# Optimization experiments

Hardware: AMD Instinct MI355X
Metric: run time of the kernel (lower is better)

The kernel has to match this reference:

```python
import jax, jax.numpy as jnp
import numpy as np

B, T, C, E, TOPK = 4, 4096, 1024, 8, 2
H = 4 * C

def setup_inputs() -> dict:
    key = jax.random.key(0)
    ks = jax.random.split(key, 8)
    s = 1.0 / np.sqrt(C)
    sh = 1.0 / np.sqrt(H)
    return {
        "x": jax.random.normal(ks[0], (B, T, C), jnp.float32),
        "noise_eps": jax.random.normal(ks[1], (B, T, E), jnp.float32),
        "route_w": jax.random.normal(ks[2], (C, E), jnp.float32) * s,
        "route_b": jnp.zeros((E,), jnp.float32),
        "noise_w": jax.random.normal(ks[3], (C, E), jnp.float32) * s,
        "noise_b": jnp.zeros((E,), jnp.float32),
        "w1": jax.random.normal(ks[4], (E, C, H), jnp.float32) * s,
        "b1": jnp.zeros((E, H), jnp.float32),
        "w2": jax.random.normal(ks[5], (E, H, C), jnp.float32) * sh,
        "b2": jnp.zeros((E, C), jnp.float32),
        "top_k": TOPK,
    }

def reference(x, noise_eps, route_w, route_b, noise_w, noise_b, w1, b1, w2, b2, top_k):
    Bq, Tq, Cq = x.shape
    nE = route_w.shape[1]
    xf = x.reshape(Bq * Tq, Cq)                      # [N, C]
    N = xf.shape[0]
    logits = xf @ route_w + route_b                   # [N, E]
    std = jax.nn.softplus(xf @ noise_w + noise_b)     # [N, E]
    noisy = logits + noise_eps.reshape(N, nE) * std   # [N, E]
    _, top_idx = jax.lax.top_k(noisy, top_k)          # [N, K]
    rows = jnp.arange(N)[:, None]
    mask = jnp.zeros((N, nE), bool).at[rows, top_idx].set(True)
    # softmax over only the selected logits (others -> prob 0)
    probs = jax.nn.softmax(jnp.where(mask, noisy, -jnp.inf), axis=-1)  # [N, E]
    out = jnp.zeros_like(xf)
    for e in range(nE):  # small fixed expert count
        h = jax.nn.relu(xf @ w1[e] + b1[e])           # [N, 4C]
        y = h @ w2[e] + b2[e]                         # [N, C]
        out = out + probs[:, e:e + 1] * y             # prob==0 for unrouted tokens
    return out.reshape(Bq, Tq, Cq)
```

## Files before the change

kernel.cpp:

```cpp
#include <hip/hip_runtime.h>
#include <hip/hip_bf16.h>
#include <stdint.h>

#define NC 1024
#define NE 8
#define NH 4096
#define NN 16384

typedef __bf16 bf16x8_t __attribute__((ext_vector_type(8)));
typedef float f32x4_t __attribute__((ext_vector_type(4)));

__device__ __forceinline__ void cvt8(const float4 a, const float4 b, __bf16* dst) {
  bf16x8_t r;
  r[0] = (__bf16)a.x; r[1] = (__bf16)a.y; r[2] = (__bf16)a.z; r[3] = (__bf16)a.w;
  r[4] = (__bf16)b.x; r[5] = (__bf16)b.y; r[6] = (__bf16)b.z; r[7] = (__bf16)b.w;
  *(bf16x8_t*)dst = r;
}

__device__ __forceinline__ void mfma_step(const __bf16* __restrict__ Asc,
    const __bf16* __restrict__ Bsc, int a_off, int b_off, f32x4_t (&acc)[4][4]) {
  bf16x8_t af[4], bfr[4];
#pragma unroll
  for (int mi = 0; mi < 4; ++mi) af[mi] = *(const bf16x8_t*)(Asc + a_off + mi * 512);
#pragma unroll
  for (int ni = 0; ni < 4; ++ni) bfr[ni] = *(const bf16x8_t*)(Bsc + b_off + ni * 512);
#pragma unroll
  for (int mi = 0; mi < 4; ++mi)
#pragma unroll
    for (int ni = 0; ni < 4; ++ni)
      acc[mi][ni] = __builtin_amdgcn_mfma_f32_16x16x32_bf16(af[mi], bfr[ni], acc[mi][ni], 0, 0, 0);
}

__global__ __launch_bounds__(256) void routing_kernel(
    const float* __restrict__ x, const float* __restrict__ eps,
    const float* __restrict__ rw, const float* __restrict__ rb,
    const float* __restrict__ nw, const float* __restrict__ nb,
    int* __restrict__ eidx, float2* __restrict__ pp2) {
  const int lane = threadIdx.x & 63;
  const int n = blockIdx.x * 4 + (threadIdx.x >> 6);
  if (n >= NN) return;
  double acc[16];
#pragma unroll
  for (int i = 0; i < 16; ++i) acc[i] = 0.0;
  const float* xr = x + (size_t)n * NC;
  for (int c0 = 0; c0 < NC; c0 += 64) {
    const int c = c0 + lane;
    const float xv = xr[c];
    const float4 r0 = *(const float4*)(rw + (size_t)c * NE);
    const float4 r1 = *(const float4*)(rw + (size_t)c * NE + 4);
    const float4 n0 = *(const float4*)(nw + (size_t)c * NE);
    const float4 n1 = *(const float4*)(nw + (size_t)c * NE + 4);
    acc[0] += (double)xv * r0.x;  acc[1] += (double)xv * r0.y;
    acc[2] += (double)xv * r0.z;  acc[3] += (double)xv * r0.w;
    acc[4] += (double)xv * r1.x;  acc[5] += (double)xv * r1.y;
    acc[6] += (double)xv * r1.z;  acc[7] += (double)xv * r1.w;
    acc[8] += (double)xv * n0.x;  acc[9] += (double)xv * n0.y;
    acc[10] += (double)xv * n0.z; acc[11] += (double)xv * n0.w;
    acc[12] += (double)xv * n1.x; acc[13] += (double)xv * n1.y;
    acc[14] += (double)xv * n1.z; acc[15] += (double)xv * n1.w;
  }
#pragma unroll
  for (int off = 32; off > 0; off >>= 1) {
#pragma unroll
    for (int i = 0; i < 16; ++i) acc[i] += __shfl_xor(acc[i], off, 64);
  }
  if (lane == 0) {
    double noisy[NE];
#pragma unroll
    for (int e = 0; e < NE; ++e) {
      const double lg = acc[e] + (double)rb[e];
      const double z = acc[8 + e] + (double)nb[e];
      const double sp = log1p(exp(-fabs(z))) + fmax(z, 0.0);
      noisy[e] = lg + (double)eps[(size_t)n * NE + e] * sp;
    }
    int i1 = -1, i2 = -1;
    double v1 = -1e300, v2 = -1e300;
#pragma unroll
    for (int e = 0; e < NE; ++e) {
      const double v = noisy[e];
      if (v > v1) { v2 = v1; i2 = i1; v1 = v; i1 = e; }
      else if (v > v2) { v2 = v; i2 = e; }
    }
    if (i1 < 0) i1 = 0;
    if (i2 < 0 || i2 == i1) i2 = (i1 + 1) & 7;
    const double d = exp(v2 - v1);
    const float p1 = (float)(1.0 / (1.0 + d));
    const float p2 = (float)(d / (1.0 + d));
    eidx[n] = i1 | (i2 << 8);
    pp2[n] = float2{p1, p2};
  }
}

__global__ __launch_bounds__(256) void build_lists(
    const int* __restrict__ eidx, const float2* __restrict__ pp2,
    int* __restrict__ counts, int* __restrict__ perm, float* __restrict__ pprob) {
  __shared__ int hist[NE];
  __shared__ int base[NE];
  const int t = threadIdx.x;
  if (t < NE) hist[t] = 0;
  __syncthreads();
  const int n = blockIdx.x * 256 + t;
  const int packed = eidx[n];
  const int e1 = packed & 255;
  const int e2 = (packed >> 8) & 255;
  const float2 p = pp2[n];
  const int l1 = atomicAdd(&hist[e1], 1);
  const int l2 = atomicAdd(&hist[e2], 1);
  __syncthreads();
  if (t < NE) base[t] = atomicAdd(&counts[t], hist[t]);
  __syncthreads();
  const int o1 = base[e1] + l1;
  const int o2 = base[e2] + l2;
  perm[e1 * NN + o1] = n; pprob[e1 * NN + o1] = p.x;
  perm[e2 * NN + o2] = n; pprob[e2 * NN + o2] = p.y;
}

__global__ __launch_bounds__(256) void transpose_cvt(
    const float* __restrict__ src, __bf16* __restrict__ dst, int R, int Cc) {
  const size_t mat = (size_t)R * Cc;
  src += (size_t)blockIdx.z * mat;
  dst += (size_t)blockIdx.z * mat;
  __shared__ __align__(16) __bf16 tile[64][72];
  const int r0 = blockIdx.y * 64, c0 = blockIdx.x * 64;
  const int t = threadIdx.x;
  const int tr = t >> 3;
  const int tc = (t & 7) * 8;
#pragma unroll
  for (int h = 0; h < 2; ++h) {
    const int r = tr + h * 32;
    const float* sp = src + (size_t)(r0 + r) * Cc + (c0 + tc);
    const float4 a = *(const float4*)sp;
    const float4 b = *(const float4*)(sp + 4);
    cvt8(a, b, &tile[r][tc]);
  }
  __syncthreads();
#pragma unroll
  for (int h = 0; h < 2; ++h) {
    const int c = tr + h * 32;
    __bf16 tmp[8] __attribute__((aligned(16)));
#pragma unroll
    for (int j = 0; j < 8; ++j) tmp[j] = tile[tc + j][c];
    __bf16* dp = dst + (size_t)(c0 + c) * R + (r0 + tc);
    *(uint4*)dp = *(const uint4*)tmp;
  }
}


template<bool FASTB>
__global__ __launch_bounds__(256) void moe_gemm1(
    const float* __restrict__ x, const void* __restrict__ bsrc,
    const float* __restrict__ bias, __bf16* __restrict__ hbuf,
    const int* __restrict__ counts_e, const int* __restrict__ perm_e, int chunk_start) {
  int cnt = *counts_e; if (cnt > NN) cnt = NN; if (cnt < 0) cnt = 0;
  const int lr0 = blockIdx.y * 128;
  const int row0 = chunk_start + lr0;
  if (row0 >= cnt) return;
  const int t = threadIdx.x;

  __shared__ __align__(16) __bf16 As[2 * 128 * 32];
  __shared__ __align__(16) __bf16 Bs[2 * 128 * 32];

  const int ar1 = row0 + (t >> 2), ar2 = ar1 + 64;
  const int tokA = (ar1 < cnt) ? perm_e[ar1] : 0;
  const int tokB = (ar2 < cnt) ? perm_e[ar2] : 0;
  const int kg = (t & 3) * 8;
  const float* pA1 = x + (size_t)tokA * NC + kg;
  const float* pA2 = x + (size_t)tokB * NC + kg;
  const int n0 = blockIdx.x * 128;

  const __bf16* pB1 = nullptr; const __bf16* pB2 = nullptr;
  const float* pBw = nullptr;
  const int kk = t >> 3, cc = (t & 7) * 16;
  if (FASTB) {
    const __bf16* bt = (const __bf16*)bsrc;
    const int nrow = n0 + (t >> 2);
    pB1 = bt + (size_t)nrow * NC + kg;
    pB2 = bt + (size_t)(nrow + 64) * NC + kg;
  } else {
    pBw = (const float*)bsrc + (size_t)kk * NH + n0 + cc;
  }

  f32x4_t acc[4][4];
#pragma unroll
  for (int i = 0; i < 4; ++i)
#pragma unroll
    for (int j = 0; j < 4; ++j)
#pragma unroll
      for (int k = 0; k < 4; ++k) acc[i][j][k] = 0.f;

  const int lane = t & 63, wid = t >> 6;
  const int wm = (wid >> 1) * 64, wn = (wid & 1) * 64;
  const int col16 = lane & 15, quad = lane >> 4;

  if (FASTB) {
    const int woff = (t >> 2) * 32 + (((t & 3) ^ ((t >> 3) & 3)) * 8);
    const int sel = (col16 >> 1) & 3;
    const int a_off = (wm + col16) * 32 + ((quad ^ sel) * 8);
    const int b_off = (wn + col16) * 32 + ((quad ^ sel) * 8);
    __bf16* As0 = As; __bf16* As1 = As + 4096;
    __bf16* Bs0 = Bs; __bf16* Bs1 = Bs + 4096;

    float4 a1a0 = *(const float4*)(pA1),      a1b0 = *(const float4*)(pA1 + 4);
    float4 a2a0 = *(const float4*)(pA2),      a2b0 = *(const float4*)(pA2 + 4);
    uint4  vb10 = *(const uint4*)(pB1),       vb20 = *(const uint4*)(pB2);
    float4 a1a1 = *(const float4*)(pA1 + 32), a1b1 = *(const float4*)(pA1 + 36);
    float4 a2a1 = *(const float4*)(pA2 + 32), a2b1 = *(const float4*)(pA2 + 36);
    uint4  vb11 = *(const uint4*)(pB1 + 32),  vb21 = *(const uint4*)(pB2 + 32);

    for (int k0 = 0; k0 < NC; k0 += 64) {
      cvt8(a1a0, a1b0, As0 + woff);
      cvt8(a2a0, a2b0, As0 + 2048 + woff);
      *(uint4*)(Bs0 + woff) = vb10;
      *(uint4*)(Bs0 + 2048 + woff) = vb20;
      {
        const int kn = (k0 + 64 < NC) ? k0 + 64 : 0;
        a1a0 = *(const float4*)(pA1 + kn); a1b0 = *(const float4*)(pA1 + kn + 4);
        a2a0 = *(const float4*)(pA2 + kn); a2b0 = *(const float4*)(pA2 + kn + 4);
        vb10 = *(const uint4*)(pB1 + kn);  vb20 = *(const uint4*)(pB2 + kn);
      }
      __syncthreads();
      mfma_step(As0, Bs0, a_off, b_off, acc);
      cvt8(a1a1, a1b1, As1 + woff);
      cvt8(a2a1, a2b1, As1 + 2048 + woff);
      *(uint4*)(Bs1 + woff) = vb11;
      *(uint4*)(Bs1 + 2048 + woff) = vb21;
      {
        const int kn = (k0 + 96 < NC) ? k0 + 96 : 0;
        a1a1 = *(const float4*)(pA1 + kn); a1b1 = *(const float4*)(pA1 + kn + 4);
        a2a1 = *(const float4*)(pA2 + kn); a2b1 = *(const float4*)(pA2 + kn + 4);
        vb11 = *(const uint4*)(pB1 + kn);  vb21 = *(const uint4*)(pB2 + kn);
      }
      __syncthreads();
      mfma_step(As1, Bs1, a_off, b_off, acc);
    }
  } else {
    const int a_off = (wm + col16) * 32 + quad * 8;
    for (int k0 = 0; k0 < NC; k0 += 32) {
      const float4 a1a = *(const float4*)(pA1 + k0);
      const float4 a1b = *(const float4*)(pA1 + k0 + 4);
      const float4 a2a = *(const float4*)(pA2 + k0);
      const float4 a2b = *(const float4*)(pA2 + k0 + 4);
      const float* pw = pBw + (size_t)k0 * NH;
      const float4 w0 = *(const float4*)pw;
      const float4 w1 = *(const float4*)(pw + 4);
      const float4 w2 = *(const float4*)(pw + 8);
      const float4 w3 = *(const float4*)(pw + 12);
      __syncthreads();
      cvt8(a1a, a1b, As + t * 8);
      cvt8(a2a, a2b, As + 2048 + t * 8);
      cvt8(w0, w1, Bs + kk * 128 + cc);
      cvt8(w2, w3, Bs + kk * 128 + cc + 8);
      __syncthreads();
      bf16x8_t af[4], bfr[4];
#pragma unroll
      for (int mi = 0; mi < 4; ++mi) af[mi] = *(const bf16x8_t*)(As + a_off + mi * 512);
#pragma unroll
      for (int ni = 0; ni < 4; ++ni) {
        const int bn = wn + ni * 16 + col16;
#pragma unroll
        for (int j = 0; j < 8; ++j) bfr[ni][j] = Bs[(quad * 8 + j) * 128 + bn];
      }
#pragma unroll
      for (int mi = 0; mi < 4; ++mi)
#pragma unroll
        for (int ni = 0; ni < 4; ++ni)
          acc[mi][ni] = __builtin_amdgcn_mfma_f32_16x16x32_bf16(af[mi], bfr[ni], acc[mi][ni], 0, 0, 0);
    }
  }

  const int colbase = n0 + wn + col16;
#pragma unroll
  for (int mi = 0; mi < 4; ++mi)
#pragma unroll
    for (int reg = 0; reg < 4; ++reg) {
      const int lr = lr0 + wm + mi * 16 + quad * 4 + reg;
      if (chunk_start + lr < cnt) {
        __bf16* hp = hbuf + (size_t)lr * NH + colbase;
#pragma unroll
        for (int ni = 0; ni < 4; ++ni) {
          const float v = acc[mi][ni][reg] + bias[colbase + ni * 16];
          hp[ni * 16] = (__bf16)fmaxf(v, 0.f);
        }
      }
    }
}

template<bool FASTB>
__global__ __launch_bounds__(256) void moe_gemm2(
    const __bf16* __restrict__ hbuf, const void* __restrict__ bsrc,
    const float* __restrict__ bias, float* __restrict__ out,
    const int* __restrict__ counts_e, const int* __restrict__ perm_e,
    const float* __restrict__ pprob_e, int chunk_start) {
  int cnt = *counts_e; if (cnt > NN) cnt = NN; if (cnt < 0) cnt = 0;
  const int lr0 = blockIdx.y * 128;
  if (chunk_start + lr0 >= cnt) return;
  const int t = threadIdx.x;

  __shared__ __align__(16) __bf16 As[2 * 128 * 32];
  __shared__ __align__(16) __bf16 Bs[2 * 128 * 32];

  const int lar1 = lr0 + (t >> 2);
  const int kg = (t & 3) * 8;
  const __bf16* pA1 = hbuf + (size_t)lar1 * NH + kg;
  const __bf16* pA2 = pA1 + (size_t)64 * NH;
  const int n0 = blockIdx.x * 128;

  const __bf16* pB1 = nullptr; const __bf16* pB2 = nullptr;
  const float* pBw = nullptr;
  const int kk = t >> 3, cc = (t & 7) * 16;
  if (FASTB) {
    const __bf16* bt = (const __bf16*)bsrc;
    const int nrow = n0 + (t >> 2);
    pB1 = bt + (size_t)nrow * NH + kg;
    pB2 = bt + (size_t)(nrow + 64) * NH + kg;
  } else {
    pBw = (const float*)bsrc + (size_t)kk * NC + n0 + cc;
  }

  f32x4_t acc[4][4];
#pragma unroll
  for (int i = 0; i < 4; ++i)
#pragma unroll
    for (int j = 0; j < 4; ++j)
#pragma unroll
      for (int k = 0; k < 4; ++k) acc[i][j][k] = 0.f;

  const int lane = t & 63, wid = t >> 6;
  const int wm = (wid >> 1) * 64, wn = (wid & 1) * 64;
  const int col16 = lane & 15, quad = lane >> 4;

  if (FASTB) {
    const int woff = (t >> 2) * 32 + (((t & 3) ^ ((t >> 3) & 3)) * 8);
    const int sel = (col16 >> 1) & 3;
    const int a_off = (wm + col16) * 32 + ((quad ^ sel) * 8);
    const int b_off = (wn + col16) * 32 + ((quad ^ sel) * 8);
    __bf16* As0 = As; __bf16* As1 = As + 4096;
    __bf16* Bs0 = Bs; __bf16* Bs1 = Bs + 4096;

    uint4 va10 = *(const uint4*)(pA1),      va20 = *(const uint4*)(pA2);
    uint4 vb10 = *(const uint4*)(pB1),      vb20 = *(const uint4*)(pB2);
    uint4 va11 = *(const uint4*)(pA1 + 32), va21 = *(const uint4*)(pA2 + 32);
    uint4 vb11 = *(const uint4*)(pB1 + 32), vb21 = *(const uint4*)(pB2 + 32);

    for (int k0 = 0; k0 < NH; k0 += 64) {
      *(uint4*)(As0 + woff) = va10;
      *(uint4*)(As0 + 2048 + woff) = va20;
      *(uint4*)(Bs0 + woff) = vb10;
      *(uint4*)(Bs0 + 2048 + woff) = vb20;
      {
        const int kn = (k0 + 64 < NH) ? k0 + 64 : 0;
        va10 = *(const uint4*)(pA1 + kn); va20 = *(const uint4*)(pA2 + kn);
        vb10 = *(const uint4*)(pB1 + kn); vb20 = *(const uint4*)(pB2 + kn);
      }
      __syncthreads();
      mfma_step(As0, Bs0, a_off, b_off, acc);
      *(uint4*)(As1 + woff) = va11;
      *(uint4*)(As1 + 2048 + woff) = va21;
      *(uint4*)(Bs1 + woff) = vb11;
      *(uint4*)(Bs1 + 2048 + woff) = vb21;
      {
        const int kn = (k0 + 96 < NH) ? k0 + 96 : 0;
        va11 = *(const uint4*)(pA1 + kn); va21 = *(const uint4*)(pA2 + kn);
        vb11 = *(const uint4*)(pB1 + kn); vb21 = *(const uint4*)(pB2 + kn);
      }
      __syncthreads();
      mfma_step(As1, Bs1, a_off, b_off, acc);
    }
  } else {
    const int a_off = (wm + col16) * 32 + quad * 8;
    for (int k0 = 0; k0 < NH; k0 += 32) {
      const uint4 va1 = *(const uint4*)(pA1 + k0);
      const uint4 va2 = *(const uint4*)(pA2 + k0);
      const float* pw = pBw + (size_t)k0 * NC;
      const float4 w0 = *(const float4*)pw;
      const float4 w1 = *(const float4*)(pw + 4);
      const float4 w2 = *(const float4*)(pw + 8);
      const float4 w3 = *(const float4*)(pw + 12);
      __syncthreads();
      *(uint4*)(As + t * 8) = va1;
      *(uint4*)(As + 2048 + t * 8) = va2;
      cvt8(w0, w1, Bs + kk * 128 + cc);
      cvt8(w2, w3, Bs + kk * 128 + cc + 8);
      __syncthreads();
      bf16x8_t af[4], bfr[4];
#pragma unroll
      for (int mi = 0; mi < 4; ++mi) af[mi] = *(const bf16x8_t*)(As + a_off + mi * 512);
#pragma unroll
      for (int ni = 0; ni < 4; ++ni) {
        const int bn = wn + ni * 16 + col16;
#pragma unroll
        for (int j = 0; j < 8; ++j) bfr[ni][j] = Bs[(quad * 8 + j) * 128 + bn];
      }
#pragma unroll
      for (int mi = 0; mi < 4; ++mi)
#pragma unroll
        for (int ni = 0; ni < 4; ++ni)
          acc[mi][ni] = __builtin_amdgcn_mfma_f32_16x16x32_bf16(af[mi], bfr[ni], acc[mi][ni], 0, 0, 0);
    }
  }

  const int colbase = n0 + wn + col16;
#pragma unroll
  for (int mi = 0; mi < 4; ++mi)
#pragma unroll
    for (int reg = 0; reg < 4; ++reg) {
      const int lr = lr0 + wm + mi * 16 + quad * 4 + reg;
      const int r = chunk_start + lr;
      if (r < cnt) {
        const int tok = perm_e[r];
        const float p = pprob_e[r];
        float* op = out + (size_t)tok * NC + colbase;
#pragma unroll
        for (int ni = 0; ni < 4; ++ni) {
          op[ni * 16] += (acc[mi][ni][reg] + bias[colbase + ni * 16]) * p;
        }
      }
    }
}

extern "C" void kernel_launch(void* const* d_in, const int* in_sizes, int n_in,
                              void* d_out, int out_size, void* d_ws, size_t ws_size,
                              hipStream_t stream) {
  (void)in_sizes; (void)n_in;
  const float* x   = (const float*)d_in[0];
  const float* eps = (const float*)d_in[1];
  const float* rw  = (const float*)d_in[2];
  const float* rb  = (const float*)d_in[3];
  const float* nw  = (const float*)d_in[4];
  const float* nb  = (const float*)d_in[5];
  const float* w1  = (const float*)d_in[6];
  const float* b1  = (const float*)d_in[7];
  const float* w2  = (const float*)d_in[8];
  const float* b2  = (const float*)d_in[9];
  float* out = (float*)d_out;

  char* wsb = (char*)d_ws;
  int* counts = (int*)wsb;
  int* perm = (int*)(wsb + 256);
  float* pprob = (float*)(wsb + 256 + (size_t)NE * NN * 4);
  int* eidx = (int*)(wsb + 256 + (size_t)NE * NN * 8);
  float2* pp2 = (float2*)(wsb + 256 + (size_t)NE * NN * 8 + (size_t)NN * 4);
  size_t off = 256 + (size_t)NE * NN * 8 + (size_t)NN * 12;

  const size_t wtile = (size_t)NC * NH * 2;
  const size_t hfull = (size_t)NN * NH * 2;
  const bool fast2 = ws_size >= off + 2 * NE * wtile + hfull + (4u << 20);
  const bool fast = fast2 ||
      ws_size >= off + 2 * wtile + (size_t)128 * NH * 2 + (1u << 20);
  __bf16* w1t = nullptr; __bf16* w2t = nullptr;
  if (fast2) {
    w1t = (__bf16*)(wsb + off); off += NE * wtile;
    w2t = (__bf16*)(wsb + off); off += NE * wtile;
  } else if (fast) {
    w1t = (__bf16*)(wsb + off); off += wtile;
    w2t = (__bf16*)(wsb + off); off += wtile;
  }
  __bf16* hbuf = (__bf16*)(wsb + off);
  const size_t remain = (ws_size > off) ? (ws_size - off) : 0;
  long rows_cap = (long)(remain / ((size_t)NH * 2));
  rows_cap = (rows_cap / 128) * 128;
  if (rows_cap > NN) rows_cap = NN;
  if (rows_cap < 128) rows_cap = 128;

  hipMemsetAsync(counts, 0, 256, stream);
  hipMemsetAsync(d_out, 0, (size_t)out_size * 4, stream);

  routing_kernel<<<NN / 4, 256, 0, stream>>>(x, eps, rw, rb, nw, nb, eidx, pp2);
  build_lists<<<NN / 256, 256, 0, stream>>>(eidx, pp2, counts, perm, pprob);

  if (fast2) {
    transpose_cvt<<<dim3(NH / 64, NC / 64, NE), 256, 0, stream>>>(w1, w1t, NC, NH);
    transpose_cvt<<<dim3(NC / 64, NH / 64, NE), 256, 0, stream>>>(w2, w2t, NH, NC);
  }

  const int nchunks = (int)((NN + rows_cap - 1) / rows_cap);
  for (int e = 0; e < NE; ++e) {
    const float* w1e = w1 + (size_t)e * NC * NH;
    const float* w2e = w2 + (size_t)e * NH * NC;
    const __bf16* w1te = fast2 ? (w1t + (size_t)e * NC * NH) : w1t;
    const __bf16* w2te = fast2 ? (w2t + (size_t)e * NH * NC) : w2t;
    if (fast && !fast2) {
      transpose_cvt<<<dim3(NH / 64, NC / 64, 1), 256, 0, stream>>>(w1e, w1t, NC, NH);
      transpose_cvt<<<dim3(NC / 64, NH / 64, 1), 256, 0, stream>>>(w2e, w2t, NH, NC);
    }
    for (int ch = 0; ch < nchunks; ++ch) {
      const int cs = ch * (int)rows_cap;
      if (fast) {
        moe_gemm1<true><<<dim3(NH / 128, (unsigned)(rows_cap / 128)), 256, 0, stream>>>(
            x, w1te, b1 + (size_t)e * NH, hbuf, counts + e, perm + (size_t)e * NN, cs);
        moe_gemm2<true><<<dim3(NC / 128, (unsigned)(rows_cap / 128)), 256, 0, stream>>>(
            hbuf, w2te, b2 + (size_t)e * NC, out, counts + e, perm + (size_t)e * NN,
            pprob + (size_t)e * NN, cs);
      } else {
        moe_gemm1<false><<<dim3(NH / 128, (unsigned)(rows_cap / 128)), 256, 0, stream>>>(
            x, w1e, b1 + (size_t)e * NH, hbuf, counts + e, perm + (size_t)e * NN, cs);
        moe_gemm2<false><<<dim3(NC / 128, (unsigned)(rows_cap / 128)), 256, 0, stream>>>(
            hbuf, w2e, b2 + (size_t)e * NC, out, counts + e, perm + (size_t)e * NN,
            pprob + (size_t)e * NN, cs);
      }
    }
  }
}
```

Baseline: 1.659 ms.

## Merge per-expert GEMM launches into single grouped launches with XCD-aware work decode

Adds grouped GEMM kernels that process all experts in one launch each for the up- and down-projections. Each block decodes its expert and row tile from the per-expert counts, and the block index is remapped so consecutive work lands on the same XCD. Hidden activations are packed contiguously across experts. This removes the per-expert launch loop and its tail underutilization, at the cost of launching many empty blocks (a fixed 264-row grid) and requiring a larger workspace.

Result: faster. 1.533 ms (-7.6%).

```diff
diff --git a/kernel.cpp b/kernel.cpp
--- a/kernel.cpp
+++ b/kernel.cpp
@@ -29,6 +29,30 @@
 #pragma unroll
     for (int ni = 0; ni < 4; ++ni)
       acc[mi][ni] = __builtin_amdgcn_mfma_f32_16x16x32_bf16(af[mi], bfr[ni], acc[mi][ni], 0, 0, 0);
+}
+
+template<int GX>
+__device__ __forceinline__ bool decode_work(const int* __restrict__ counts,
+    int& e, int& lr0, int& cnt, int& hbase, int& n0) {
+  const int nwg = GX * (int)gridDim.y;
+  const int lin = (int)blockIdx.y * GX + (int)blockIdx.x;
+  const int q = nwg >> 3, r = nwg & 7;
+  const int xcd = lin & 7, idx = lin >> 3;
+  const int work = (xcd < r) ? (xcd * (q + 1) + idx)
+                             : (r * (q + 1) + (xcd - r) * q + idx);
+  const int wx = work & (GX - 1);
+  const int wy = work / GX;
+  n0 = wx * 128;
+  e = -1; lr0 = 0; cnt = 0; hbase = 0;
+  int pc = 0, hc = 0;
+#pragma unroll
+  for (int i = 0; i < NE; ++i) {
+    int ci = counts[i]; ci = ci < 0 ? 0 : (ci > NN ? NN : ci);
+    const int pb = (ci + 127) >> 7;
+    if (e < 0 && wy < pc + pb) { e = i; lr0 = (wy - pc) * 128; cnt = ci; hbase = hc; }
+    pc += pb; hc += ci;
+  }
+  return (e >= 0) && (lr0 < cnt);
 }
 
 __global__ __launch_bounds__(256) void routing_kernel(
@@ -146,6 +170,191 @@
 }
 
 
+template<int GX>
+__global__ __launch_bounds__(256) void moe_gemm1f(
+    const float* __restrict__ x, const __bf16* __restrict__ w1t_all,
+    const float* __restrict__ b1_all, __bf16* __restrict__ hbuf,
+    const int* __restrict__ counts, const int* __restrict__ perm) {
+  int e, lr0, cnt, hbase, n0;
+  if (!decode_work<GX>(counts, e, lr0, cnt, hbase, n0)) return;
+  const int t = threadIdx.x;
+  const int* perm_e = perm + e * NN;
+  const __bf16* bt = w1t_all + (size_t)e * NC * NH;
+  const float* bias = b1_all + (size_t)e * NH;
+
+  __shared__ __align__(16) __bf16 As[2 * 128 * 32];
+  __shared__ __align__(16) __bf16 Bs[2 * 128 * 32];
+
+  const int ar1 = lr0 + (t >> 2), ar2 = ar1 + 64;
+  const int tokA = (ar1 < cnt) ? perm_e[ar1] : 0;
+  const int tokB = (ar2 < cnt) ? perm_e[ar2] : 0;
+  const int kg = (t & 3) * 8;
+  const float* pA1 = x + (size_t)tokA * NC + kg;
+  const float* pA2 = x + (size_t)tokB * NC + kg;
+  const int nrow = n0 + (t >> 2);
+  const __bf16* pB1 = bt + (size_t)nrow * NC + kg;
+  const __bf16* pB2 = bt + (size_t)(nrow + 64) * NC + kg;
+
+  f32x4_t acc[4][4];
+#pragma unroll
+  for (int i = 0; i < 4; ++i)
+#pragma unroll
+    for (int j = 0; j < 4; ++j)
+#pragma unroll
+      for (int k = 0; k < 4; ++k) acc[i][j][k] = 0.f;
+
+  const int lane = t & 63, wid = t >> 6;
+  const int wm = (wid >> 1) * 64, wn = (wid & 1) * 64;
+  const int col16 = lane & 15, quad = lane >> 4;
+  const int woff = (t >> 2) * 32 + (((t & 3) ^ ((t >> 3) & 3)) * 8);
+  const int sel = (col16 >> 1) & 3;
+  const int a_off = (wm + col16) * 32 + ((quad ^ sel) * 8);
+  const int b_off = (wn + col16) * 32 + ((quad ^ sel) * 8);
+  __bf16* As0 = As; __bf16* As1 = As + 4096;
+  __bf16* Bs0 = Bs; __bf16* Bs1 = Bs + 4096;
+
+  float4 a1a0 = *(const float4*)(pA1),      a1b0 = *(const float4*)(pA1 + 4);
+  float4 a2a0 = *(const float4*)(pA2),      a2b0 = *(const float4*)(pA2 + 4);
+  uint4  vb10 = *(const uint4*)(pB1),       vb20 = *(const uint4*)(pB2);
+  float4 a1a1 = *(const float4*)(pA1 + 32), a1b1 = *(const float4*)(pA1 + 36);
+  float4 a2a1 = *(const float4*)(pA2 + 32), a2b1 = *(const float4*)(pA2 + 36);
+  uint4  vb11 = *(const uint4*)(pB1 + 32),  vb21 = *(const uint4*)(pB2 + 32);
+
+  for (int k0 = 0; k0 < NC; k0 += 64) {
+    cvt8(a1a0, a1b0, As0 + woff);
+    cvt8(a2a0, a2b0, As0 + 2048 + woff);
+    *(uint4*)(Bs0 + woff) = vb10;
+    *(uint4*)(Bs0 + 2048 + woff) = vb20;
+    {
+      const int kn = (k0 + 64 < NC) ? k0 + 64 : 0;
+      a1a0 = *(const float4*)(pA1 + kn); a1b0 = *(const float4*)(pA1 + kn + 4);
+      a2a0 = *(const float4*)(pA2 + kn); a2b0 = *(const float4*)(pA2 + kn + 4);
+      vb10 = *(const uint4*)(pB1 + kn);  vb20 = *(const uint4*)(pB2 + kn);
+    }
+    __syncthreads();
+    mfma_step(As0, Bs0, a_off, b_off, acc);
+    cvt8(a1a1, a1b1, As1 + woff);
+    cvt8(a2a1, a2b1, As1 + 2048 + woff);
+    *(uint4*)(Bs1 + woff) = vb11;
+    *(uint4*)(Bs1 + 2048 + woff) = vb21;
+    {
+      const int kn = (k0 + 96 < NC) ? k0 + 96 : 0;
+      a1a1 = *(const float4*)(pA1 + kn); a1b1 = *(const float4*)(pA1 + kn + 4);
+      a2a1 = *(const float4*)(pA2 + kn); a2b1 = *(const float4*)(pA2 + kn + 4);
+      vb11 = *(const uint4*)(pB1 + kn);  vb21 = *(const uint4*)(pB2 + kn);
+    }
+    __syncthreads();
+    mfma_step(As1, Bs1, a_off, b_off, acc);
+  }
+
+  const int colbase = n0 + wn + col16;
+#pragma unroll
+  for (int mi = 0; mi < 4; ++mi)
+#pragma unroll
+    for (int reg = 0; reg < 4; ++reg) {
+      const int lr = lr0 + wm + mi * 16 + quad * 4 + reg;
+      if (lr < cnt) {
+        __bf16* hp = hbuf + (size_t)(hbase + lr) * NH + colbase;
+#pragma unroll
+        for (int ni = 0; ni < 4; ++ni) {
+          const float v = acc[mi][ni][reg] + bias[colbase + ni * 16];
+          hp[ni * 16] = (__bf16)fmaxf(v, 0.f);
+        }
+      }
+    }
+}
+
+template<int GX>
+__global__ __launch_bounds__(256) void moe_gemm2f(
+    const __bf16* __restrict__ hbuf, const __bf16* __restrict__ w2t_all,
+    const float* __restrict__ b2_all, float* __restrict__ out,
+    const int* __restrict__ counts, const int* __restrict__ perm,
+    const float* __restrict__ pprob) {
+  int e, lr0, cnt, hbase, n0;
+  if (!decode_work<GX>(counts, e, lr0, cnt, hbase, n0)) return;
+  const int t = threadIdx.x;
+  const int* perm_e = perm + e * NN;
+  const float* pprob_e = pprob + e * NN;
+  const __bf16* bt = w2t_all + (size_t)e * NH * NC;
+  const float* bias = b2_all + (size_t)e * NC;
+
+  __shared__ __align__(16) __bf16 As[2 * 128 * 32];
+  __shared__ __align__(16) __bf16 Bs[2 * 128 * 32];
+
+  const int lar1 = lr0 + (t >> 2);
+  const int kg = (t & 3) * 8;
+  const __bf16* pA1 = hbuf + (size_t)(hbase + lar1) * NH + kg;
+  const __bf16* pA2 = pA1 + (size_t)64 * NH;
+  const int nrow = n0 + (t >> 2);
+  const __bf16* pB1 = bt + (size_t)nrow * NH + kg;
+  const __bf16* pB2 = bt + (size_t)(nrow + 64) * NH + kg;
+
+  f32x4_t acc[4][4];
+#pragma unroll
+  for (int i = 0; i < 4; ++i)
+#pragma unroll
+    for (int j = 0; j < 4; ++j)
+#pragma unroll
+      for (int k = 0; k < 4; ++k) acc[i][j][k] = 0.f;
+
+  const int lane = t & 63, wid = t >> 6;
+  const int wm = (wid >> 1) * 64, wn = (wid & 1) * 64;
+  const int col16 = lane & 15, quad = lane >> 4;
+  const int woff = (t >> 2) * 32 + (((t & 3) ^ ((t >> 3) & 3)) * 8);
+  const int sel = (col16 >> 1) & 3;
+  const int a_off = (wm + col16) * 32 + ((quad ^ sel) * 8);
+  const int b_off = (wn + col16) * 32 + ((quad ^ sel) * 8);
+  __bf16* As0 = As; __bf16* As1 = As + 4096;
+  __bf16* Bs0 = Bs; __bf16* Bs1 = Bs + 4096;
+
+  uint4 va10 = *(const uint4*)(pA1),      va20 = *(const uint4*)(pA2);
+  uint4 vb10 = *(const uint4*)(pB1),      vb20 = *(const uint4*)(pB2);
+  uint4 va11 = *(const uint4*)(pA1 + 32), va21 = *(const uint4*)(pA2 + 32);
+  uint4 vb11 = *(const uint4*)(pB1 + 32), vb21 = *(const uint4*)(pB2 + 32);
+
+  for (int k0 = 0; k0 < NH; k0 += 64) {
+    *(uint4*)(As0 + woff) = va10;
+    *(uint4*)(As0 + 2048 + woff) = va20;
+    *(uint4*)(Bs0 + woff) = vb10;
+    *(uint4*)(Bs0 + 2048 + woff) = vb20;
+    {
+      const int kn = (k0 + 64 < NH) ? k0 + 64 : 0;
+      va10 = *(const uint4*)(pA1 + kn); va20 = *(const uint4*)(pA2 + kn);
+      vb10 = *(const uint4*)(pB1 + kn); vb20 = *(const uint4*)(pB2 + kn);
+    }
+    __syncthreads();
+    mfma_step(As0, Bs0, a_off, b_off, acc);
+    *(uint4*)(As1 + woff) = va11;
+    *(uint4*)(As1 + 2048 + woff) = va21;
+    *(uint4*)(Bs1 + woff) = vb11;
+    *(uint4*)(Bs1 + 2048 + woff) = vb21;
+    {
+      const int kn = (k0 + 96 < NH) ? k0 + 96 : 0;
+      va11 = *(const uint4*)(pA1 + kn); va21 = *(const uint4*)(pA2 + kn);
+      vb11 = *(const uint4*)(pB1 + kn); vb21 = *(const uint4*)(pB2 + kn);
+    }
+    __syncthreads();
+    mfma_step(As1, Bs1, a_off, b_off, acc);
+  }
+
+  const int colbase = n0 + wn + col16;
+#pragma unroll
+  for (int mi = 0; mi < 4; ++mi)
+#pragma unroll
+    for (int reg = 0; reg < 4; ++reg) {
+      const int lr = lr0 + wm + mi * 16 + quad * 4 + reg;
+      if (lr < cnt) {
+        const int tok = perm_e[lr];
+        const float p = pprob_e[lr];
+        float* op = out + (size_t)tok * NC + colbase;
+#pragma unroll
+        for (int ni = 0; ni < 4; ++ni) {
+          atomicAdd(op + ni * 16, (acc[mi][ni][reg] + bias[colbase + ni * 16]) * p);
+        }
+      }
+    }
+}
+
 template<bool FASTB>
 __global__ __launch_bounds__(256) void moe_gemm1(
     const float* __restrict__ x, const void* __restrict__ bsrc,
@@ -443,8 +652,11 @@
   size_t off = 256 + (size_t)NE * NN * 8 + (size_t)NN * 12;
 
   const size_t wtile = (size_t)NC * NH * 2;
+  const size_t hpack = (size_t)(2 * NN + 256) * NH * 2;
   const size_t hfull = (size_t)NN * NH * 2;
-  const bool fast2 = ws_size >= off + 2 * NE * wtile + hfull + (4u << 20);
+  const bool fusedmode = ws_size >= off + 2 * NE * wtile + hpack + (1u << 20);
+  const bool fast2 = fusedmode ||
+      ws_size >= off + 2 * NE * wtile + hfull + (4u << 20);
   const bool fast = fast2 ||
       ws_size >= off + 2 * wtile + (size_t)128 * NH * 2 + (1u << 20);
   __bf16* w1t = nullptr; __bf16* w2t = nullptr;
@@ -467,6 +679,14 @@
 
   routing_kernel<<<NN / 4, 256, 0, stream>>>(x, eps, rw, rb, nw, nb, eidx, pp2);
   build_lists<<<NN / 256, 256, 0, stream>>>(eidx, pp2, counts, perm, pprob);
+
+  if (fusedmode) {
+    transpose_cvt<<<dim3(NH / 64, NC / 64, NE), 256, 0, stream>>>(w1, w1t, NC, NH);
+    transpose_cvt<<<dim3(NC / 64, NH / 64, NE), 256, 0, stream>>>(w2, w2t, NH, NC);
+    moe_gemm1f<32><<<dim3(32, 264), 256, 0, stream>>>(x, w1t, b1, hbuf, counts, perm);
+    moe_gemm2f<8><<<dim3(8, 264), 256, 0, stream>>>(hbuf, w2t, b2, out, counts, perm, pprob);
+    return;
+  }
 
   if (fast2) {
     transpose_cvt<<<dim3(NH / 64, NC / 64, NE), 256, 0, stream>>>(w1, w1t, NC, NH);
```
